# Kernel tuning notes

Measured on AMD Instinct MI355X. Metric: run time of the kernel, lower is better.

The kernel has to match this reference:

```python
import jax, jax.numpy as jnp
import numpy as np
from jax import lax

BN_EPS = 1e-5  # eval-mode BatchNorm with running_mean=0, running_var=1


def _interp_mat(n_in, n_out):
    # align_corners=True bilinear interpolation matrix [n_out, n_in]
    if n_out == 1:
        coords = np.zeros((1,))
    else:
        coords = np.arange(n_out) * (n_in - 1) / (n_out - 1)
    lo = np.clip(np.floor(coords).astype(np.int64), 0, max(n_in - 2, 0))
    frac = (coords - lo).astype(np.float32)
    M = np.zeros((n_out, n_in), dtype=np.float32)
    M[np.arange(n_out), lo] += 1.0 - frac
    if n_in > 1:
        M[np.arange(n_out), lo + 1] += frac
    return jnp.asarray(M)


def _resize_ac(x, H, W):
    # bilinear, align_corners=True, over trailing two dims
    Mh = _interp_mat(x.shape[-2], H)
    Mw = _interp_mat(x.shape[-1], W)
    return jnp.einsum('...hw,Hh,Ww->...HW', x, Mh, Mw)


def _conv(x, w, b, pad):
    y = lax.conv_general_dilated(x, w, (1, 1), [(pad, pad), (pad, pad)],
                                 dimension_numbers=('NCHW', 'OIHW', 'NCHW'))
    return y + b[None, :, None, None]


def setup_inputs() -> dict:
    key = jax.random.key(0)
    ks = jax.random.split(key, 16)
    C, KD, VD, NCLS, BS = 256, 32, 128, 10, 4
    sizes = [64, 32, 16, 8, 4]
    inp = {}
    for l, s in enumerate(sizes):
        inp[f'feat{l}'] = jax.random.normal(ks[l], (BS, C, s, s), jnp.float32)
    inp['attentions'] = jax.random.normal(ks[5], (NCLS, C, 16, 16), jnp.float32)

    def w(k, shape):
        return jax.random.normal(k, shape, jnp.float32) * 0.05

    inp['key_t_w'] = w(ks[6], (KD, C, 3, 3)); inp['key_t_b'] = jnp.zeros((KD,), jnp.float32)
    inp['value_t_w'] = w(ks[7], (VD, C, 3, 3)); inp['value_t_b'] = jnp.zeros((VD,), jnp.float32)
    inp['key_q_w'] = w(ks[8], (5, KD, C, 3, 3)); inp['key_q_b'] = jnp.zeros((5, KD), jnp.float32)
    inp['value_q_w'] = w(ks[9], (5, VD, C, 3, 3)); inp['value_q_b'] = jnp.zeros((5, VD), jnp.float32)
    inp['bn_gamma'] = jnp.ones((5, 256), jnp.float32)
    inp['bn_beta'] = jnp.zeros((5, 256), jnp.float32)
    inp['combine_w'] = w(ks[10], (256, 512, 1, 1)); inp['combine_b'] = jnp.zeros((256,), jnp.float32)
    return inp


def reference(feat0, feat1, feat2, feat3, feat4, attentions,
              key_t_w, key_t_b, value_t_w, value_t_b,
              key_q_w, key_q_b, value_q_w, value_q_b,
              bn_gamma, bn_beta, combine_w, combine_b):
    feats = [feat0, feat1, feat2, feat3, feat4]
    ncls, _, h, w_ = attentions.shape
    hw = h * w_
    kt = _conv(attentions, key_t_w, key_t_b, 1).reshape(ncls, 32, hw)   # [n,32,hw]
    vt = _conv(attentions, value_t_w, value_t_b, 1).reshape(ncls, 128, hw)  # [n,128,hw]
    bn_scale = bn_gamma * np.float32(1.0 / np.sqrt(1.0 + BN_EPS))
    outs, fas = [], []
    for l, f in enumerate(feats):
        bs, _, H, W = f.shape
        fr = _resize_ac(f, h, w_)                                        # [b,C,h,w]
        kq = _conv(fr, key_q_w[l], key_q_b[l], 1).reshape(bs, 32, hw)    # [b,32,hw]
        vq = _conv(fr, value_q_w[l], value_q_b[l], 1)                    # [b,128,h,w]
        # p[b,n,i,j] = sum_k kq[b,k,i] * kt[n,k,j]; softmax over i (torch dim=1)
        p = jnp.einsum('bki,nkj->bnij', kq, kt)
        p = jax.nn.softmax(p, axis=2)
        # full attention maps: channels = template pixel j, spatial = query pixel i
        fa = _resize_ac(jnp.swapaxes(p, 2, 3).reshape(bs, ncls, hw, h, w_), H, W)
        # val_t_out summed over classes: sum_n sum_i vt[n,c,i] * p[b,n,i,j]
        agg = jnp.einsum('nci,bnij->bcj', vt, p).reshape(bs, 128, h, w_)
        final = jnp.concatenate([ncls * vq, agg], axis=1)                # [b,256,h,w]
        final = _resize_ac(final, H, W)
        final = final * bn_scale[l][None, :, None, None] + bn_beta[l][None, :, None, None]
        outs.append(_conv(jnp.concatenate([f, final], axis=1), combine_w, combine_b, 0))
        fas.append(fa)
    return (*outs, *fas)
```

## Files before the change

kernel.cpp:

```cpp
#include <hip/hip_runtime.h>

constexpr int CIN   = 256;
constexpr int KD    = 32;
constexpr int VD    = 128;
constexpr int NCLS  = 10;
constexpr int BS    = 4;
constexpr int HW    = 256;
constexpr float BNC = 0.9999950000374997f;

typedef unsigned short u16;
typedef __attribute__((ext_vector_type(8))) __bf16 bf8v;
typedef __attribute__((ext_vector_type(4))) float f4v;

static __device__ __forceinline__ int imin(int a, int b) { return a < b ? a : b; }

static __device__ __forceinline__ u16 f2bf(float v) {
  union { float f; unsigned u; } x; x.f = v;
  unsigned r = x.u + 0x7FFFu + ((x.u >> 16) & 1u);
  return (u16)(r >> 16);
}
static __device__ __forceinline__ float bf2f(u16 h) {
  union { unsigned u; float f; } x; x.u = ((unsigned)h) << 16;
  return x.f;
}

static __device__ __forceinline__ f4v mfma16(bf8v a, bf8v b, f4v c) {
  return __builtin_amdgcn_mfma_f32_16x16x32_bf16(a, b, c, 0, 0, 0);
}

__constant__ const int c_jbase[5] = {0, 16384, 20480, 21504, 21760};

__global__ __launch_bounds__(256) void k_prep_f(
    const float* __restrict__ f0, const float* __restrict__ f1,
    const float* __restrict__ f2, const float* __restrict__ f3,
    const float* __restrict__ f4, const float* __restrict__ att,
    u16* __restrict__ Xf, u16* __restrict__ Xr) {
  int blk = blockIdx.x;
  const float* fin; u16* dstbase; int SS, px0;
  if (blk < 344) {
    int l, base, nb;
    if (blk < 256)      { l = 0; base = 0;   nb = 64; }
    else if (blk < 320) { l = 1; base = 256; nb = 16; }
    else if (blk < 336) { l = 2; base = 320; nb = 4; }
    else if (blk < 340) { l = 3; base = 336; nb = 1; }
    else                { l = 4; base = 340; nb = 1; }
    int local = blk - base;
    int b = local / nb, chunk = local % nb;
    int S = 64 >> l; SS = S * S;
    px0 = chunk * 64;
    fin = (l == 0 ? f0 : l == 1 ? f1 : l == 2 ? f2 : l == 3 ? f3 : f4)
          + (size_t)b * CIN * SS;
    dstbase = Xf + (size_t)(c_jbase[l] + b * SS) * 512;
  } else {
    int a = blk - 344;
    int imgA = a >> 2, chunk = a & 3;
    SS = 256; px0 = chunk * 64;
    fin = att + (size_t)imgA * CIN * 256;
    dstbase = Xr + (size_t)(20 + imgA) * 131072;
  }
  int tid = threadIdx.x;
  __shared__ float sm[16][65];
  int px_r = tid & 63, cr = tid >> 6;
  int px_w = tid >> 2, c4 = (tid & 3) * 4;
  for (int cbk = 0; cbk < 16; ++cbk) {
    __syncthreads();
#pragma unroll
    for (int q = 0; q < 4; ++q) {
      int cl = q * 4 + cr;
      float v = 0.f;
      if (px0 + px_r < SS) v = fin[(size_t)(cbk * 16 + cl) * SS + px0 + px_r];
      sm[cl][px_r] = v;
    }
    __syncthreads();
    if (px0 + px_w < SS) {
      u16 hh[4], ll[4];
#pragma unroll
      for (int e = 0; e < 4; ++e) {
        float v = sm[c4 + e][px_w];
        hh[e] = f2bf(v); ll[e] = f2bf(v - bf2f(hh[e]));
      }
      uint2 wh, wl;
      wh.x = (unsigned)hh[0] | ((unsigned)hh[1] << 16); wh.y = (unsigned)hh[2] | ((unsigned)hh[3] << 16);
      wl.x = (unsigned)ll[0] | ((unsigned)ll[1] << 16); wl.y = (unsigned)ll[2] | ((unsigned)ll[3] << 16);
      u16* dst = dstbase + (size_t)(px0 + px_w) * 512 + cbk * 16 + c4;
      *reinterpret_cast<uint2*>(dst) = wh;
      *reinterpret_cast<uint2*>(dst + 256) = wl;
    }
  }
}

__global__ __launch_bounds__(256) void k_prep_xr(
    const u16* __restrict__ Xf, u16* __restrict__ Xr, u16* __restrict__ zrow) {
  int blk = blockIdx.x;
  int img = blk >> 4, yr = blk & 15;
  int l = img >> 2, b = img & 3;
  int S = 64 >> l, SS = S * S;
  int c = threadIdx.x;
  if (blk == 0) { zrow[c] = 0; zrow[256 + c] = 0; }
  float cyf = (float)(yr * (S - 1)) / 15.0f;
  int ylo = imin((int)cyf, S - 2); float fy = cyf - (float)ylo;
  u16* dst = Xr + ((size_t)img * 256 + yr * 16) * 512;
  const u16* srcb = Xf + (size_t)(c_jbase[l] + b * SS) * 512;
  for (int x = 0; x < 16; ++x) {
    float cxf = (float)(x * (S - 1)) / 15.0f;
    int xlo = imin((int)cxf, S - 2); float fx = cxf - (float)xlo;
    const u16* r00 = srcb + (size_t)(ylo * S + xlo) * 512;
    const u16* r10 = srcb + (size_t)((ylo + 1) * S + xlo) * 512;
    float v00 = bf2f(r00[c]) + bf2f(r00[256 + c]);
    float v01 = bf2f(r00[512 + c]) + bf2f(r00[768 + c]);
    float v10 = bf2f(r10[c]) + bf2f(r10[256 + c]);
    float v11 = bf2f(r10[512 + c]) + bf2f(r10[768 + c]);
    float v = (1.f - fy) * ((1.f - fx) * v00 + fx * v01)
            + fy * ((1.f - fx) * v10 + fx * v11);
    u16 h = f2bf(v);
    dst[x * 512 + c] = h;
    dst[x * 512 + 256 + c] = f2bf(v - bf2f(h));
  }
}

__global__ __launch_bounds__(256) void k_prep_w(
    const float* __restrict__ vqw, const float* __restrict__ vtw,
    const float* __restrict__ kqw, const float* __restrict__ ktw,
    u16* __restrict__ Awv, u16* __restrict__ Awk) {
  int gid = blockIdx.x * 256 + threadIdx.x;
  int lane = gid & 63;
  int grp = gid >> 6;
  const float* src; u16* dst; int kc;
  if (grp < 3456) {
    kc = grp % 72; int ot = (grp / 72) % 8; int sid = grp / (72 * 8);
    src = (sid < 5 ? vqw + (size_t)sid * VD * 2304 : vtw) + (size_t)(ot * 16 + (lane & 15)) * 2304;
    dst = Awv + (size_t)grp * 1024;
  } else {
    int g2 = grp - 3456;
    kc = g2 % 72; int ot = (g2 / 72) % 2; int sid = g2 / 144;
    src = (sid < 5 ? kqw + (size_t)sid * KD * 2304 : ktw) + (size_t)(ot * 16 + (lane & 15)) * 2304;
    dst = Awk + (size_t)g2 * 1024;
  }
  int q0 = (lane >> 4) * 8;
  int t = kc >> 3, c0 = (kc & 7) * 32;
#pragma unroll
  for (int i = 0; i < 8; ++i) {
    int c = c0 + q0 + i;
    float v = src[c * 9 + t];
    u16 h = f2bf(v);
    dst[lane * 8 + i] = h;
    dst[512 + lane * 8 + i] = f2bf(v - bf2f(h));
  }
}

__global__ __launch_bounds__(256) void k_prep_cwg(
    const float* __restrict__ cw, const float* __restrict__ gamma,
    u16* __restrict__ cwA, u16* __restrict__ cw2A) {
  int blk = blockIdx.x;
  if (blk < 64) {
    int gid = blk * 256 + threadIdx.x;
    int oc = gid >> 6, c0 = (gid & 63) * 4;
    float4 v = *reinterpret_cast<const float4*>(cw + (size_t)oc * 512 + c0);
    const float* vv = (const float*)&v;
    u16 h[4], l[4];
#pragma unroll
    for (int e = 0; e < 4; ++e) { h[e] = f2bf(vv[e]); l[e] = f2bf(vv[e] - bf2f(h[e])); }
    uint2 wh, wl;
    wh.x = (unsigned)h[0] | ((unsigned)h[1] << 16); wh.y = (unsigned)h[2] | ((unsigned)h[3] << 16);
    wl.x = (unsigned)l[0] | ((unsigned)l[1] << 16); wl.y = (unsigned)l[2] | ((unsigned)l[3] << 16);
    *reinterpret_cast<uint2*>(cwA + (size_t)oc * 256 + c0) = wh;
    *reinterpret_cast<uint2*>(cwA + 65536 + (size_t)oc * 256 + c0) = wl;
  } else {
    int gid = (blk - 64) * 256 + threadIdx.x;
    int l = gid / 16384, rem = gid % 16384;
    int oc = rem >> 6, c0 = (rem & 63) * 4;
    u16 h[4], lo[4];
#pragma unroll
    for (int e = 0; e < 4; ++e) {
      int c = c0 + e;
      float v = cw[(size_t)oc * 512 + 256 + c] * (gamma[l * 256 + c] * BNC);
      h[e] = f2bf(v); lo[e] = f2bf(v - bf2f(h[e]));
    }
    uint2 wh, wl;
    wh.x = (unsigned)h[0] | ((unsigned)h[1] << 16); wh.y = (unsigned)h[2] | ((unsigned)h[3] << 16);
    wl.x = (unsigned)lo[0] | ((unsigned)lo[1] << 16); wl.y = (unsigned)lo[2] | ((unsigned)lo[3] << 16);
    *reinterpret_cast<uint2*>(cw2A + (size_t)l * 65536 + oc * 256 + c0) = wh;
    *reinterpret_cast<uint2*>(cw2A + 327680 + (size_t)l * 65536 + oc * 256 + c0) = wl;
  }
}

__global__ __launch_bounds__(256) void k_cb(
    const float* __restrict__ cw, const float* __restrict__ cbias,
    const float* __restrict__ beta, float* __restrict__ cb) {
  int l = blockIdx.x, oc = threadIdx.x;
  float s = cbias[oc];
  for (int c = 0; c < CIN; ++c)
    s += cw[(size_t)oc * 512 + 256 + c] * beta[l * CIN + c];
  cb[l * CIN + oc] = s;
}

__global__ __launch_bounds__(256) void k_conv_mfma(
    const u16* __restrict__ Xr, const u16* __restrict__ Awv, const u16* __restrict__ Awk,
    const u16* __restrict__ zrow,
    float* __restrict__ kqall, float* __restrict__ vt, float* __restrict__ f16v,
    const float* __restrict__ vqb, const float* __restrict__ vtb,
    const float* __restrict__ kqb, const float* __restrict__ ktb) {
  int wid = blockIdx.x * 4 + (threadIdx.x >> 6);
  int lane = threadIdx.x & 63;
  bool isV = wid < 1920;
  int img, ot, yp;
  if (isV) { img = wid >> 6; int r = wid & 63; ot = r >> 3; yp = r & 7; }
  else     { int j = wid - 1920; img = j >> 4; int r = j & 15; ot = r >> 3; yp = r & 7; }
  int wset = img < 20 ? (img >> 2) : 5;

  const u16* Ab = isV ? Awv + ((size_t)(wset * 8 + ot)) * 72 * 1024
                      : Awk + ((size_t)(wset * 2 + ot)) * 72 * 1024;
  const u16* Xb = Xr + (size_t)img * 131072;
  int xcol = lane & 15, kg = lane >> 4;
  int y0 = yp * 2, y1 = y0 + 1;

  f4v acc0 = {0.f, 0.f, 0.f, 0.f}, acc1 = {0.f, 0.f, 0.f, 0.f};
  for (int t = 0; t < 9; ++t) {
    int dy = (t >= 6) ? 2 : (t >= 3 ? 1 : 0);
    int dx = t - dy * 3;
    int yy0 = y0 + dy - 1, yy1 = yy0 + 1;
    int xx = xcol + dx - 1;
    bool xok = (unsigned)xx < 16u;
    const u16* base0 = (xok && (unsigned)yy0 < 16u)
                       ? Xb + (size_t)(yy0 * 16 + xx) * 512 : zrow;
    const u16* base1 = (xok && (unsigned)yy1 < 16u)
                       ? Xb + (size_t)(yy1 * 16 + xx) * 512 : zrow;
    const u16* Xr0 = base0 + kg * 8;
    const u16* Xr1 = base1 + kg * 8;
    const u16* Ak = Ab + (size_t)t * 8 * 1024 + lane * 8;
#pragma unroll
    for (int cc = 0; cc < 8; ++cc) {
      bf8v ah = *reinterpret_cast<const bf8v*>(Ak + cc * 1024);
      bf8v al = *reinterpret_cast<const bf8v*>(Ak + cc * 1024 + 512);
      bf8v bh0 = *reinterpret_cast<const bf8v*>(Xr0 + cc * 32);
      bf8v bl0 = *reinterpret_cast<const bf8v*>(Xr0 + cc * 32 + 256);
      bf8v bh1 = *reinterpret_cast<const bf8v*>(Xr1 + cc * 32);
      bf8v bl1 = *reinterpret_cast<const bf8v*>(Xr1 + cc * 32 + 256);
      acc0 = mfma16(ah, bh0, acc0);
      acc0 = mfma16(ah, bl0, acc0);
      acc0 = mfma16(al, bh0, acc0);
      acc1 = mfma16(ah, bh1, acc1);
      acc1 = mfma16(ah, bl1, acc1);
      acc1 = mfma16(al, bh1, acc1);
    }
  }

  float scale = 1.f;
  const float* bias;
  float* dst;
  int ocbase = ot * 16;
  if (isV) {
    if (img < 20) { dst = f16v + ((size_t)img * VD + ocbase) * HW; bias = vqb + wset * VD + ocbase; scale = (float)NCLS; }
    else          { dst = vt + ((size_t)(img - 20) * VD + ocbase) * HW; bias = vtb + ocbase; }
  } else {
    if (img < 20) { dst = kqall + ((size_t)img * KD + ocbase) * HW; bias = kqb + wset * KD + ocbase; }
    else          { dst = kqall + (size_t)20 * KD * HW + ((size_t)(img - 20) * KD + ocbase) * HW; bias = ktb + ocbase; }
  }
#pragma unroll
  for (int i = 0; i < 4; ++i) {
    int ocl = kg * 4 + i;
    float bv = bias[ocl];
    dst[(size_t)ocl * HW + y0 * 16 + xcol] = (acc0[i] + bv) * scale;
    dst[(size_t)ocl * HW + y1 * 16 + xcol] = (acc1[i] + bv) * scale;
  }
}

__global__ __launch_bounds__(256) void k_prep_vt(
    const float* __restrict__ vt, u16* __restrict__ vt2) {
  int gid = blockIdx.x * 256 + threadIdx.x;
  float4 v = *reinterpret_cast<const float4*>(vt + (size_t)gid * 4);
  const float* vv = (const float*)&v;
  u16 h[4], l[4];
#pragma unroll
  for (int e = 0; e < 4; ++e) { h[e] = f2bf(vv[e]); l[e] = f2bf(vv[e] - bf2f(h[e])); }
  uint2 wh, wl;
  wh.x = (unsigned)h[0] | ((unsigned)h[1] << 16); wh.y = (unsigned)h[2] | ((unsigned)h[3] << 16);
  wl.x = (unsigned)l[0] | ((unsigned)l[1] << 16); wl.y = (unsigned)l[2] | ((unsigned)l[3] << 16);
  *reinterpret_cast<uint2*>(vt2 + (size_t)gid * 4) = wh;
  *reinterpret_cast<uint2*>(vt2 + 327680 + (size_t)gid * 4) = wl;
}

__global__ __launch_bounds__(256) void k_mega(
    const float* __restrict__ kqall, const u16* __restrict__ vt2,
    float* __restrict__ out, float* __restrict__ aggn) {
  int blk = blockIdx.x;
  int l = blk / 160;
  int r = blk % 160;
  int b = r / 40;
  int r2 = r % 40;
  int np = r2 >> 3, jt = r2 & 7;
  int t = threadIdx.x;
  int iq = t >> 5, jl = t & 31;
  int j = jt * 32 + jl;

  __shared__ float buf[8224];
  __shared__ float red[512];

  const float* ktb = kqall + 20 * KD * HW;
  const float* kqb = kqall + (size_t)(l * 4 + b) * KD * HW;

  int S_ = 64 >> l, shift = 6 - l, SS = S_ * S_;
  const size_t fa_off[5] = {5586944, 47529984, 58015744, 60637184, 61292544};

  int w = t >> 6, lane = t & 63;
  int row = lane & 15, kg = lane >> 4;
  f4v acc[2][2] = {{{0.f,0.f,0.f,0.f},{0.f,0.f,0.f,0.f}},
                   {{0.f,0.f,0.f,0.f},{0.f,0.f,0.f,0.f}}};

  for (int half = 0; half < 2; ++half) {
    int n = np * 2 + half;
    int bn = b * NCLS + n;
    __syncthreads();
    for (int s = t; s < KD * HW; s += 256) buf[s] = kqb[s];
    float ktr[KD];
#pragma unroll
    for (int k = 0; k < KD; ++k) ktr[k] = ktb[((size_t)n * KD + k) * HW + j];
    __syncthreads();

    float v[32];
#pragma unroll
    for (int ii = 0; ii < 32; ++ii) v[ii] = 0.f;
    for (int k = 0; k < KD; ++k) {
      float a = ktr[k];
      const float4* q4 = (const float4*)&buf[k * 256 + iq * 32];
#pragma unroll
      for (int q = 0; q < 8; ++q) {
        float4 u = q4[q];
        v[q * 4 + 0] += u.x * a; v[q * 4 + 1] += u.y * a;
        v[q * 4 + 2] += u.z * a; v[q * 4 + 3] += u.w * a;
      }
    }
    float ml = -1e30f;
#pragma unroll
    for (int ii = 0; ii < 32; ++ii) ml = fmaxf(ml, v[ii]);
    float sl = 0.f;
#pragma unroll
    for (int ii = 0; ii < 32; ++ii) sl += __expf(v[ii] - ml);
    red[t] = ml;
    red[256 + t] = sl;
    __syncthreads();
    float M = -1e30f;
#pragma unroll
    for (int q = 0; q < 8; ++q) M = fmaxf(M, red[q * 32 + jl]);
    float Ssum = 0.f;
#pragma unroll
    for (int q = 0; q < 8; ++q) Ssum += red[256 + q * 32 + jl] * __expf(red[q * 32 + jl] - M);
    float inv = 1.0f / Ssum;
#pragma unroll
    for (int ii = 0; ii < 32; ++ii)
      buf[jl * 257 + iq * 32 + ii] = __expf(v[ii] - M) * inv;
    __syncthreads();

    float* ob = out + fa_off[l] + ((size_t)bn * HW + jt * 32) * SS;
    int tot = SS << 5;
    for (int base = t * 4; base < tot; base += 1024) {
      int jj = base >> (2 * shift);
      int rest = base & (SS - 1);
      int X0 = rest & (S_ - 1), Y = rest >> shift;
      float cyf = (float)(Y * 15) / (float)(S_ - 1);
      int ylo = imin((int)cyf, 14); float fy = cyf - (float)ylo;
      const float* prow = &buf[jj * 257];
      float4 rv; float* rr = (float*)&rv;
#pragma unroll
      for (int t4 = 0; t4 < 4; ++t4) {
        int X = X0 + t4;
        float cxf = (float)(X * 15) / (float)(S_ - 1);
        int xlo = imin((int)cxf, 14); float fx = cxf - (float)xlo;
        int i00 = ylo * 16 + xlo;
        float v0 = prow[i00],      v1 = prow[i00 + 1];
        float v2 = prow[i00 + 16], v3 = prow[i00 + 17];
        rr[t4] = (1.f - fy) * ((1.f - fx) * v0 + fx * v1)
               + fy * ((1.f - fx) * v2 + fx * v3);
      }
      *(float4*)(ob + (size_t)jj * SS + rest) = rv;
    }

    for (int kc = 0; kc < 8; ++kc) {
      bf8v ah[2], al[2];
#pragma unroll
      for (int ctl = 0; ctl < 2; ++ctl) {
        int ct = w * 2 + ctl;
        const u16* vh = vt2 + ((size_t)n * VD + ct * 16 + row) * 256 + kc * 32 + kg * 8;
        ah[ctl] = *reinterpret_cast<const bf8v*>(vh);
        al[ctl] = *reinterpret_cast<const bf8v*>(vh + 327680);
      }
#pragma unroll
      for (int jt2 = 0; jt2 < 2; ++jt2) {
        union { u16 u[8]; bf8v v8; } Bh, Bl;
#pragma unroll
        for (int e = 0; e < 8; ++e) {
          float f = buf[(jt2 * 16 + row) * 257 + kc * 32 + kg * 8 + e];
          u16 h = f2bf(f);
          Bh.u[e] = h; Bl.u[e] = f2bf(f - bf2f(h));
        }
#pragma unroll
        for (int ctl = 0; ctl < 2; ++ctl) {
          acc[ctl][jt2] = mfma16(ah[ctl], Bh.v8, acc[ctl][jt2]);
          acc[ctl][jt2] = mfma16(ah[ctl], Bl.v8, acc[ctl][jt2]);
          acc[ctl][jt2] = mfma16(al[ctl], Bh.v8, acc[ctl][jt2]);
        }
      }
    }
  }

  float* ab = aggn + (size_t)(l * 20 + b * 5 + np) * VD * HW;
#pragma unroll
  for (int ctl = 0; ctl < 2; ++ctl)
#pragma unroll
    for (int jt2 = 0; jt2 < 2; ++jt2)
#pragma unroll
      for (int i = 0; i < 4; ++i)
        ab[(size_t)(w * 32 + ctl * 16 + kg * 4 + i) * HW + jt * 32 + jt2 * 16 + row]
            = acc[ctl][jt2][i];
}

__global__ __launch_bounds__(256) void k_fuse_fs(
    const float* __restrict__ f16v, const float* __restrict__ aggn,
    u16* __restrict__ fsT) {
  int blk = blockIdx.x;
  int img = blk >> 4, jc = blk & 15;
  int j0 = jc * 16;
  int l = img >> 2, b = img & 3;
  int tid = threadIdx.x;
  __shared__ float fs[256][17];
  for (int pass = 0; pass < 16; ++pass) {
    int cc = pass * 16 + (tid >> 4);
    int jj = tid & 15;
    float v;
    if (cc < 128) {
      v = f16v[((size_t)img * VD + cc) * HW + j0 + jj];
    } else {
      const float* ab = aggn + ((size_t)(l * 20 + b * 5) * VD + cc - 128) * HW + j0 + jj;
      v = 0.f;
#pragma unroll
      for (int npx = 0; npx < 5; ++npx) v += ab[(size_t)npx * VD * HW];
    }
    fs[cc][jj] = v;
  }
  __syncthreads();
  int j = tid >> 4, cg = (tid & 15) * 16;
  u16* dst = fsT + ((size_t)img * 256 + j0 + j) * 512 + cg;
#pragma unroll
  for (int e = 0; e < 16; ++e) {
    float v = fs[cg + e][j];
    u16 h = f2bf(v);
    dst[e] = h;
    dst[256 + e] = f2bf(v - bf2f(h));
  }
}

__global__ __launch_bounds__(256) void k_g16_mfma(
    const u16* __restrict__ cw2A, const u16* __restrict__ fsT,
    float* __restrict__ g16_all) {
  int wid = blockIdx.x * 4 + (threadIdx.x >> 6);
  int lane = threadIdx.x & 63;
  int img = wid >> 8;
  int r = wid & 255;
  int octile = r >> 4, jt = r & 15;
  int l = img >> 2;
  int row = lane & 15, kg = lane >> 4;
  const u16* Ah = cw2A + (size_t)l * 65536 + (octile * 16 + row) * 256 + kg * 8;
  const u16* Al = Ah + 327680;
  const u16* Bh = fsT + ((size_t)img * 256 + jt * 16 + row) * 512 + kg * 8;
  const u16* Bl = Bh + 256;
  f4v acc = {0.f, 0.f, 0.f, 0.f};
#pragma unroll
  for (int kc = 0; kc < 8; ++kc) {
    bf8v ah = *reinterpret_cast<const bf8v*>(Ah + kc * 32);
    bf8v al = *reinterpret_cast<const bf8v*>(Al + kc * 32);
    bf8v bh = *reinterpret_cast<const bf8v*>(Bh + kc * 32);
    bf8v bl = *reinterpret_cast<const bf8v*>(Bl + kc * 32);
    acc = mfma16(ah, bh, acc);
    acc = mfma16(ah, bl, acc);
    acc = mfma16(al, bh, acc);
  }
#pragma unroll
  for (int i = 0; i < 4; ++i)
    g16_all[((size_t)img * CIN + octile * 16 + kg * 4 + i) * HW + jt * 16 + row] = acc[i];
}

__global__ __launch_bounds__(256) void k_out_final(
    const u16* __restrict__ cwA, const u16* __restrict__ Xf,
    const float* __restrict__ g16_all, const float* __restrict__ cb_all,
    float* __restrict__ out) {
  int wid = blockIdx.x * 4 + (threadIdx.x >> 6);
  int lane = threadIdx.x & 63;
  int pt = wid >> 4, octile = wid & 15;
  int l, lb, tl;
  if (pt < 1024)      { l = 0; lb = 0;    tl = 256; }
  else if (pt < 1280) { l = 1; lb = 1024; tl = 64; }
  else if (pt < 1344) { l = 2; lb = 1280; tl = 16; }
  else if (pt < 1360) { l = 3; lb = 1344; tl = 4; }
  else                { l = 4; lb = 1360; tl = 1; }
  int rem = pt - lb;
  int b = rem / tl;
  int pxin = (rem % tl) * 16;
  const size_t ooff[5] = {0, 4194304, 5242880, 5505024, 5570560};
  int S = 64 >> l, SS = S * S, shift = 6 - l;
  int row = lane & 15, kg = lane >> 4;
  int gpx = c_jbase[l] + b * SS + pxin + row;

  const u16* Ah = cwA + ((size_t)(octile * 16 + row)) * 256 + kg * 8;
  const u16* Al = Ah + 65536;
  const u16* Bh = Xf + (size_t)gpx * 512 + kg * 8;
  const u16* Bl = Bh + 256;
  f4v acc = {0.f, 0.f, 0.f, 0.f};
#pragma unroll
  for (int kc = 0; kc < 8; ++kc) {
    bf8v ah = *reinterpret_cast<const bf8v*>(Ah + kc * 32);
    bf8v al = *reinterpret_cast<const bf8v*>(Al + kc * 32);
    bf8v bh = *reinterpret_cast<const bf8v*>(Bh + kc * 32);
    bf8v bl = *reinterpret_cast<const bf8v*>(Bl + kc * 32);
    acc = mfma16(ah, bh, acc);
    acc = mfma16(ah, bl, acc);
    acc = mfma16(al, bh, acc);
  }

  int px = pxin + row;
  int Xc = px & (S - 1), Y = px >> shift;
  float cyf = (float)(Y * 15) / (float)(S - 1);
  int ylo = imin((int)cyf, 14); float fy = cyf - (float)ylo;
  float cxf = (float)(Xc * 15) / (float)(S - 1);
  int xlo = imin((int)cxf, 14); float fx = cxf - (float)xlo;
  int i00 = ylo * 16 + xlo;
  const float* gbase = g16_all + ((size_t)(l * 4 + b) * CIN + octile * 16 + kg * 4) * HW;
  float* ob = out + ooff[l] + ((size_t)b * CIN + octile * 16) * SS + px;
#pragma unroll
  for (int i = 0; i < 4; ++i) {
    const float* g = gbase + (size_t)i * HW + i00;
    float v0 = g[0], v1 = g[1], v2 = g[16], v3 = g[17];
    float bil = (1.f - fy) * ((1.f - fx) * v0 + fx * v1)
              + fy * ((1.f - fx) * v2 + fx * v3);
    ob[(size_t)(kg * 4 + i) * SS] = acc[i] + bil + cb_all[l * CIN + octile * 16 + kg * 4 + i];
  }
}

extern "C" void kernel_launch(void* const* d_in, const int* in_sizes, int n_in,
                              void* d_out, int out_size, void* d_ws, size_t ws_size,
                              hipStream_t stream) {
  const float* feat[5];
  for (int l = 0; l < 5; ++l) feat[l] = (const float*)d_in[l];
  const float* att   = (const float*)d_in[5];
  const float* ktw   = (const float*)d_in[6];
  const float* ktb   = (const float*)d_in[7];
  const float* vtw   = (const float*)d_in[8];
  const float* vtb   = (const float*)d_in[9];
  const float* kqw   = (const float*)d_in[10];
  const float* kqb   = (const float*)d_in[11];
  const float* vqw   = (const float*)d_in[12];
  const float* vqb   = (const float*)d_in[13];
  const float* gamma = (const float*)d_in[14];
  const float* beta  = (const float*)d_in[15];
  const float* cw    = (const float*)d_in[16];
  const float* cbias = (const float*)d_in[17];
  float* out = (float*)d_out;

  float* ws    = (float*)d_ws;
  float* kqall = ws;
  float* f16v  = ws + 245760;
  u16*   vt2   = (u16*)(ws + 901120);
  u16*   cwA   = (u16*)(ws + 1228800);
  u16*   cw2A  = (u16*)(ws + 1294336);
  float* cb    = ws + 1622016;
  u16*   Xf    = (u16*)(ws + 1623296);
  float* S0    = ws + 7210240;
  u16*   Awv  = (u16*)S0;
  u16*   Awk  = (u16*)(S0 + 1769472);
  u16*   Xr   = (u16*)(S0 + 2211840);
  float* vt   = S0 + 4177920;
  u16*   zrow = (u16*)(S0 + 4505600);
  float* aggn    = S0;
  u16*   fsT     = (u16*)(S0 + 3276800);
  float* g16_all = S0;

  k_prep_f<<<384, 256, 0, stream>>>(
      feat[0], feat[1], feat[2], feat[3], feat[4], att, Xf, Xr);
  k_prep_w<<<1080, 256, 0, stream>>>(vqw, vtw, kqw, ktw, Awv, Awk);
  k_prep_cwg<<<384, 256, 0, stream>>>(cw, gamma, cwA, cw2A);
  k_cb<<<5, 256, 0, stream>>>(cw, cbias, beta, cb);
  k_prep_xr<<<320, 256, 0, stream>>>(Xf, Xr, zrow);
  k_conv_mfma<<<600, 256, 0, stream>>>(
      Xr, Awv, Awk, zrow, kqall, vt, f16v, vqb, vtb, kqb, ktb);
  k_prep_vt<<<320, 256, 0, stream>>>(vt, vt2);

  k_mega<<<800, 256, 0, stream>>>(kqall, vt2, out, aggn);
  k_fuse_fs<<<320, 256, 0, stream>>>(f16v, aggn, fsT);

  k_g16_mfma<<<1280, 256, 0, stream>>>(cw2A, fsT, g16_all);
  k_out_final<<<5456, 256, 0, stream>>>(cwA, Xf, g16_all, cb, out);
}
```

Baseline: 403.5 us.

## Merge prep kernels, fuse vt split into conv epilogue, one class per mega block

Four weight and feature prep kernels are merged into one launch, and the separate fp32-to-bf16 hi/lo split of the template values is moved into the conv epilogue, which drops a kernel and an intermediate buffer. k_mega now handles one class per block with twice as many blocks instead of looping over two classes, giving more parallelism. The cost is a larger aggn buffer (10 partial sums per image instead of 5) that k_fuse_fs must read and reduce, which adds memory traffic and requires moving the workspace layout.

```diff
diff --git a/kernel.cpp b/kernel.cpp
--- a/kernel.cpp
+++ b/kernel.cpp
@@ -30,62 +30,133 @@
 
 __constant__ const int c_jbase[5] = {0, 16384, 20480, 21504, 21760};
 
-__global__ __launch_bounds__(256) void k_prep_f(
+__global__ __launch_bounds__(256) void k_prep1(
     const float* __restrict__ f0, const float* __restrict__ f1,
     const float* __restrict__ f2, const float* __restrict__ f3,
     const float* __restrict__ f4, const float* __restrict__ att,
-    u16* __restrict__ Xf, u16* __restrict__ Xr) {
+    const float* __restrict__ vqw, const float* __restrict__ vtw,
+    const float* __restrict__ kqw, const float* __restrict__ ktw,
+    const float* __restrict__ cw, const float* __restrict__ gamma,
+    const float* __restrict__ cbias, const float* __restrict__ beta,
+    u16* __restrict__ Xf, u16* __restrict__ Xr,
+    u16* __restrict__ Awv, u16* __restrict__ Awk,
+    u16* __restrict__ cwA, u16* __restrict__ cw2A, float* __restrict__ cb) {
+  __shared__ float sm[16][65];
   int blk = blockIdx.x;
-  const float* fin; u16* dstbase; int SS, px0;
-  if (blk < 344) {
-    int l, base, nb;
-    if (blk < 256)      { l = 0; base = 0;   nb = 64; }
-    else if (blk < 320) { l = 1; base = 256; nb = 16; }
-    else if (blk < 336) { l = 2; base = 320; nb = 4; }
-    else if (blk < 340) { l = 3; base = 336; nb = 1; }
-    else                { l = 4; base = 340; nb = 1; }
-    int local = blk - base;
-    int b = local / nb, chunk = local % nb;
-    int S = 64 >> l; SS = S * S;
-    px0 = chunk * 64;
-    fin = (l == 0 ? f0 : l == 1 ? f1 : l == 2 ? f2 : l == 3 ? f3 : f4)
-          + (size_t)b * CIN * SS;
-    dstbase = Xf + (size_t)(c_jbase[l] + b * SS) * 512;
-  } else {
-    int a = blk - 344;
-    int imgA = a >> 2, chunk = a & 3;
-    SS = 256; px0 = chunk * 64;
-    fin = att + (size_t)imgA * CIN * 256;
-    dstbase = Xr + (size_t)(20 + imgA) * 131072;
-  }
   int tid = threadIdx.x;
-  __shared__ float sm[16][65];
-  int px_r = tid & 63, cr = tid >> 6;
-  int px_w = tid >> 2, c4 = (tid & 3) * 4;
-  for (int cbk = 0; cbk < 16; ++cbk) {
-    __syncthreads();
-#pragma unroll
-    for (int q = 0; q < 4; ++q) {
-      int cl = q * 4 + cr;
-      float v = 0.f;
-      if (px0 + px_r < SS) v = fin[(size_t)(cbk * 16 + cl) * SS + px0 + px_r];
-      sm[cl][px_r] = v;
-    }
-    __syncthreads();
-    if (px0 + px_w < SS) {
-      u16 hh[4], ll[4];
+  if (blk < 384) {
+    const float* fin; u16* dstbase; int SS, px0;
+    if (blk < 344) {
+      int l, base, nb;
+      if (blk < 256)      { l = 0; base = 0;   nb = 64; }
+      else if (blk < 320) { l = 1; base = 256; nb = 16; }
+      else if (blk < 336) { l = 2; base = 320; nb = 4; }
+      else if (blk < 340) { l = 3; base = 336; nb = 1; }
+      else                { l = 4; base = 340; nb = 1; }
+      int local = blk - base;
+      int b = local / nb, chunk = local % nb;
+      int S = 64 >> l; SS = S * S;
+      px0 = chunk * 64;
+      fin = (l == 0 ? f0 : l == 1 ? f1 : l == 2 ? f2 : l == 3 ? f3 : f4)
+            + (size_t)b * CIN * SS;
+      dstbase = Xf + (size_t)(c_jbase[l] + b * SS) * 512;
+    } else {
+      int a = blk - 344;
+      int imgA = a >> 2, chunk = a & 3;
+      SS = 256; px0 = chunk * 64;
+      fin = att + (size_t)imgA * CIN * 256;
+      dstbase = Xr + (size_t)(20 + imgA) * 131072;
+    }
+    int px_r = tid & 63, cr = tid >> 6;
+    int px_w = tid >> 2, c4 = (tid & 3) * 4;
+    for (int cbk = 0; cbk < 16; ++cbk) {
+      __syncthreads();
+#pragma unroll
+      for (int q = 0; q < 4; ++q) {
+        int cl = q * 4 + cr;
+        float v = 0.f;
+        if (px0 + px_r < SS) v = fin[(size_t)(cbk * 16 + cl) * SS + px0 + px_r];
+        sm[cl][px_r] = v;
+      }
+      __syncthreads();
+      if (px0 + px_w < SS) {
+        u16 hh[4], ll[4];
+#pragma unroll
+        for (int e = 0; e < 4; ++e) {
+          float v = sm[c4 + e][px_w];
+          hh[e] = f2bf(v); ll[e] = f2bf(v - bf2f(hh[e]));
+        }
+        uint2 wh, wl;
+        wh.x = (unsigned)hh[0] | ((unsigned)hh[1] << 16); wh.y = (unsigned)hh[2] | ((unsigned)hh[3] << 16);
+        wl.x = (unsigned)ll[0] | ((unsigned)ll[1] << 16); wl.y = (unsigned)ll[2] | ((unsigned)ll[3] << 16);
+        u16* dst = dstbase + (size_t)(px0 + px_w) * 512 + cbk * 16 + c4;
+        *reinterpret_cast<uint2*>(dst) = wh;
+        *reinterpret_cast<uint2*>(dst + 256) = wl;
+      }
+    }
+  } else if (blk < 1464) {
+    int gid = (blk - 384) * 256 + tid;
+    int lane = gid & 63;
+    int grp = gid >> 6;
+    const float* src; u16* dst; int kc;
+    if (grp < 3456) {
+      kc = grp % 72; int ot = (grp / 72) % 8; int sid = grp / (72 * 8);
+      src = (sid < 5 ? vqw + (size_t)sid * VD * 2304 : vtw) + (size_t)(ot * 16 + (lane & 15)) * 2304;
+      dst = Awv + (size_t)grp * 1024;
+    } else {
+      int g2 = grp - 3456;
+      kc = g2 % 72; int ot = (g2 / 72) % 2; int sid = g2 / 144;
+      src = (sid < 5 ? kqw + (size_t)sid * KD * 2304 : ktw) + (size_t)(ot * 16 + (lane & 15)) * 2304;
+      dst = Awk + (size_t)g2 * 1024;
+    }
+    int q0 = (lane >> 4) * 8;
+    int t = kc >> 3, c0 = (kc & 7) * 32;
+#pragma unroll
+    for (int i = 0; i < 8; ++i) {
+      int c = c0 + q0 + i;
+      float v = src[c * 9 + t];
+      u16 h = f2bf(v);
+      dst[lane * 8 + i] = h;
+      dst[512 + lane * 8 + i] = f2bf(v - bf2f(h));
+    }
+  } else if (blk < 1848) {
+    int blk2 = blk - 1464;
+    if (blk2 < 64) {
+      int gid = blk2 * 256 + tid;
+      int oc = gid >> 6, c0 = (gid & 63) * 4;
+      float4 v = *reinterpret_cast<const float4*>(cw + (size_t)oc * 512 + c0);
+      const float* vv = (const float*)&v;
+      u16 h[4], l[4];
+#pragma unroll
+      for (int e = 0; e < 4; ++e) { h[e] = f2bf(vv[e]); l[e] = f2bf(vv[e] - bf2f(h[e])); }
+      uint2 wh, wl;
+      wh.x = (unsigned)h[0] | ((unsigned)h[1] << 16); wh.y = (unsigned)h[2] | ((unsigned)h[3] << 16);
+      wl.x = (unsigned)l[0] | ((unsigned)l[1] << 16); wl.y = (unsigned)l[2] | ((unsigned)l[3] << 16);
+      *reinterpret_cast<uint2*>(cwA + (size_t)oc * 256 + c0) = wh;
+      *reinterpret_cast<uint2*>(cwA + 65536 + (size_t)oc * 256 + c0) = wl;
+    } else {
+      int gid = (blk2 - 64) * 256 + tid;
+      int l = gid / 16384, rem = gid % 16384;
+      int oc = rem >> 6, c0 = (rem & 63) * 4;
+      u16 h[4], lo[4];
 #pragma unroll
       for (int e = 0; e < 4; ++e) {
-        float v = sm[c4 + e][px_w];
-        hh[e] = f2bf(v); ll[e] = f2bf(v - bf2f(hh[e]));
+        int c = c0 + e;
+        float v = cw[(size_t)oc * 512 + 256 + c] * (gamma[l * 256 + c] * BNC);
+        h[e] = f2bf(v); lo[e] = f2bf(v - bf2f(h[e]));
       }
       uint2 wh, wl;
-      wh.x = (unsigned)hh[0] | ((unsigned)hh[1] << 16); wh.y = (unsigned)hh[2] | ((unsigned)hh[3] << 16);
-      wl.x = (unsigned)ll[0] | ((unsigned)ll[1] << 16); wl.y = (unsigned)ll[2] | ((unsigned)ll[3] << 16);
-      u16* dst = dstbase + (size_t)(px0 + px_w) * 512 + cbk * 16 + c4;
-      *reinterpret_cast<uint2*>(dst) = wh;
-      *reinterpret_cast<uint2*>(dst + 256) = wl;
-    }
+      wh.x = (unsigned)h[0] | ((unsigned)h[1] << 16); wh.y = (unsigned)h[2] | ((unsigned)h[3] << 16);
+      wl.x = (unsigned)lo[0] | ((unsigned)lo[1] << 16); wl.y = (unsigned)lo[2] | ((unsigned)lo[3] << 16);
+      *reinterpret_cast<uint2*>(cw2A + (size_t)l * 65536 + oc * 256 + c0) = wh;
+      *reinterpret_cast<uint2*>(cw2A + 327680 + (size_t)l * 65536 + oc * 256 + c0) = wl;
+    }
+  } else {
+    int l = blk - 1848, oc = tid;
+    float s = cbias[oc];
+    for (int c = 0; c < CIN; ++c)
+      s += cw[(size_t)oc * 512 + 256 + c] * beta[l * CIN + c];
+    cb[l * CIN + oc] = s;
   }
 }
 
@@ -118,86 +189,10 @@
   }
 }
 
-__global__ __launch_bounds__(256) void k_prep_w(
-    const float* __restrict__ vqw, const float* __restrict__ vtw,
-    const float* __restrict__ kqw, const float* __restrict__ ktw,
-    u16* __restrict__ Awv, u16* __restrict__ Awk) {
-  int gid = blockIdx.x * 256 + threadIdx.x;
-  int lane = gid & 63;
-  int grp = gid >> 6;
-  const float* src; u16* dst; int kc;
-  if (grp < 3456) {
-    kc = grp % 72; int ot = (grp / 72) % 8; int sid = grp / (72 * 8);
-    src = (sid < 5 ? vqw + (size_t)sid * VD * 2304 : vtw) + (size_t)(ot * 16 + (lane & 15)) * 2304;
-    dst = Awv + (size_t)grp * 1024;
-  } else {
-    int g2 = grp - 3456;
-    kc = g2 % 72; int ot = (g2 / 72) % 2; int sid = g2 / 144;
-    src = (sid < 5 ? kqw + (size_t)sid * KD * 2304 : ktw) + (size_t)(ot * 16 + (lane & 15)) * 2304;
-    dst = Awk + (size_t)g2 * 1024;
-  }
-  int q0 = (lane >> 4) * 8;
-  int t = kc >> 3, c0 = (kc & 7) * 32;
-#pragma unroll
-  for (int i = 0; i < 8; ++i) {
-    int c = c0 + q0 + i;
-    float v = src[c * 9 + t];
-    u16 h = f2bf(v);
-    dst[lane * 8 + i] = h;
-    dst[512 + lane * 8 + i] = f2bf(v - bf2f(h));
-  }
-}
-
-__global__ __launch_bounds__(256) void k_prep_cwg(
-    const float* __restrict__ cw, const float* __restrict__ gamma,
-    u16* __restrict__ cwA, u16* __restrict__ cw2A) {
-  int blk = blockIdx.x;
-  if (blk < 64) {
-    int gid = blk * 256 + threadIdx.x;
-    int oc = gid >> 6, c0 = (gid & 63) * 4;
-    float4 v = *reinterpret_cast<const float4*>(cw + (size_t)oc * 512 + c0);
-    const float* vv = (const float*)&v;
-    u16 h[4], l[4];
-#pragma unroll
-    for (int e = 0; e < 4; ++e) { h[e] = f2bf(vv[e]); l[e] = f2bf(vv[e] - bf2f(h[e])); }
-    uint2 wh, wl;
-    wh.x = (unsigned)h[0] | ((unsigned)h[1] << 16); wh.y = (unsigned)h[2] | ((unsigned)h[3] << 16);
-    wl.x = (unsigned)l[0] | ((unsigned)l[1] << 16); wl.y = (unsigned)l[2] | ((unsigned)l[3] << 16);
-    *reinterpret_cast<uint2*>(cwA + (size_t)oc * 256 + c0) = wh;
-    *reinterpret_cast<uint2*>(cwA + 65536 + (size_t)oc * 256 + c0) = wl;
-  } else {
-    int gid = (blk - 64) * 256 + threadIdx.x;
-    int l = gid / 16384, rem = gid % 16384;
-    int oc = rem >> 6, c0 = (rem & 63) * 4;
-    u16 h[4], lo[4];
-#pragma unroll
-    for (int e = 0; e < 4; ++e) {
-      int c = c0 + e;
-      float v = cw[(size_t)oc * 512 + 256 + c] * (gamma[l * 256 + c] * BNC);
-      h[e] = f2bf(v); lo[e] = f2bf(v - bf2f(h[e]));
-    }
-    uint2 wh, wl;
-    wh.x = (unsigned)h[0] | ((unsigned)h[1] << 16); wh.y = (unsigned)h[2] | ((unsigned)h[3] << 16);
-    wl.x = (unsigned)lo[0] | ((unsigned)lo[1] << 16); wl.y = (unsigned)lo[2] | ((unsigned)lo[3] << 16);
-    *reinterpret_cast<uint2*>(cw2A + (size_t)l * 65536 + oc * 256 + c0) = wh;
-    *reinterpret_cast<uint2*>(cw2A + 327680 + (size_t)l * 65536 + oc * 256 + c0) = wl;
-  }
-}
-
-__global__ __launch_bounds__(256) void k_cb(
-    const float* __restrict__ cw, const float* __restrict__ cbias,
-    const float* __restrict__ beta, float* __restrict__ cb) {
-  int l = blockIdx.x, oc = threadIdx.x;
-  float s = cbias[oc];
-  for (int c = 0; c < CIN; ++c)
-    s += cw[(size_t)oc * 512 + 256 + c] * beta[l * CIN + c];
-  cb[l * CIN + oc] = s;
-}
-
 __global__ __launch_bounds__(256) void k_conv_mfma(
     const u16* __restrict__ Xr, const u16* __restrict__ Awv, const u16* __restrict__ Awk,
     const u16* __restrict__ zrow,
-    float* __restrict__ kqall, float* __restrict__ vt, float* __restrict__ f16v,
+    float* __restrict__ kqall, u16* __restrict__ vt2, float* __restrict__ f16v,
     const float* __restrict__ vqb, const float* __restrict__ vtb,
     const float* __restrict__ kqb, const float* __restrict__ ktb) {
   int wid = blockIdx.x * 4 + (threadIdx.x >> 6);
@@ -245,17 +240,29 @@
     }
   }
 
+  int ocbase = ot * 16;
+  if (isV && img >= 20) {
+    int n = img - 20;
+    u16* d2 = vt2 + ((size_t)n * VD + ocbase) * HW;
+#pragma unroll
+    for (int i = 0; i < 4; ++i) {
+      int ocl = kg * 4 + i;
+      float bv = vtb[ocbase + ocl];
+      float va = acc0[i] + bv, vb = acc1[i] + bv;
+      u16 ha = f2bf(va), hb = f2bf(vb);
+      size_t ia = (size_t)ocl * HW + y0 * 16 + xcol;
+      size_t ib = (size_t)ocl * HW + y1 * 16 + xcol;
+      d2[ia] = ha; d2[ia + 327680] = f2bf(va - bf2f(ha));
+      d2[ib] = hb; d2[ib + 327680] = f2bf(vb - bf2f(hb));
+    }
+    return;
+  }
   float scale = 1.f;
   const float* bias;
   float* dst;
-  int ocbase = ot * 16;
-  if (isV) {
-    if (img < 20) { dst = f16v + ((size_t)img * VD + ocbase) * HW; bias = vqb + wset * VD + ocbase; scale = (float)NCLS; }
-    else          { dst = vt + ((size_t)(img - 20) * VD + ocbase) * HW; bias = vtb + ocbase; }
-  } else {
-    if (img < 20) { dst = kqall + ((size_t)img * KD + ocbase) * HW; bias = kqb + wset * KD + ocbase; }
-    else          { dst = kqall + (size_t)20 * KD * HW + ((size_t)(img - 20) * KD + ocbase) * HW; bias = ktb + ocbase; }
-  }
+  if (isV) { dst = f16v + ((size_t)img * VD + ocbase) * HW; bias = vqb + wset * VD + ocbase; scale = (float)NCLS; }
+  else if (img < 20) { dst = kqall + ((size_t)img * KD + ocbase) * HW; bias = kqb + wset * KD + ocbase; }
+  else { dst = kqall + (size_t)20 * KD * HW + ((size_t)(img - 20) * KD + ocbase) * HW; bias = ktb + ocbase; }
 #pragma unroll
   for (int i = 0; i < 4; ++i) {
     int ocl = kg * 4 + i;
@@ -265,30 +272,14 @@
   }
 }
 
-__global__ __launch_bounds__(256) void k_prep_vt(
-    const float* __restrict__ vt, u16* __restrict__ vt2) {
-  int gid = blockIdx.x * 256 + threadIdx.x;
-  float4 v = *reinterpret_cast<const float4*>(vt + (size_t)gid * 4);
-  const float* vv = (const float*)&v;
-  u16 h[4], l[4];
-#pragma unroll
-  for (int e = 0; e < 4; ++e) { h[e] = f2bf(vv[e]); l[e] = f2bf(vv[e] - bf2f(h[e])); }
-  uint2 wh, wl;
-  wh.x = (unsigned)h[0] | ((unsigned)h[1] << 16); wh.y = (unsigned)h[2] | ((unsigned)h[3] << 16);
-  wl.x = (unsigned)l[0] | ((unsigned)l[1] << 16); wl.y = (unsigned)l[2] | ((unsigned)l[3] << 16);
-  *reinterpret_cast<uint2*>(vt2 + (size_t)gid * 4) = wh;
-  *reinterpret_cast<uint2*>(vt2 + 327680 + (size_t)gid * 4) = wl;
-}
-
 __global__ __launch_bounds__(256) void k_mega(
     const float* __restrict__ kqall, const u16* __restrict__ vt2,
     float* __restrict__ out, float* __restrict__ aggn) {
   int blk = blockIdx.x;
-  int l = blk / 160;
-  int r = blk % 160;
-  int b = r / 40;
-  int r2 = r % 40;
-  int np = r2 >> 3, jt = r2 & 7;
+  int l = blk / 320;
+  int r = blk % 320;
+  int bn = r >> 3, jt = r & 7;
+  int b = bn / NCLS, n = bn % NCLS;
   int t = threadIdx.x;
   int iq = t >> 5, jl = t & 31;
   int j = jt * 32 + jl;
@@ -297,113 +288,104 @@
   __shared__ float red[512];
 
   const float* ktb = kqall + 20 * KD * HW;
+  float ktr[KD];
+#pragma unroll
+  for (int k = 0; k < KD; ++k) ktr[k] = ktb[((size_t)n * KD + k) * HW + j];
   const float* kqb = kqall + (size_t)(l * 4 + b) * KD * HW;
+  for (int s = t; s < KD * HW; s += 256) buf[s] = kqb[s];
+  __syncthreads();
+
+  float v[32];
+#pragma unroll
+  for (int ii = 0; ii < 32; ++ii) v[ii] = 0.f;
+  for (int k = 0; k < KD; ++k) {
+    float a = ktr[k];
+    const float4* q4 = (const float4*)&buf[k * 256 + iq * 32];
+#pragma unroll
+    for (int q = 0; q < 8; ++q) {
+      float4 u = q4[q];
+      v[q * 4 + 0] += u.x * a; v[q * 4 + 1] += u.y * a;
+      v[q * 4 + 2] += u.z * a; v[q * 4 + 3] += u.w * a;
+    }
+  }
+  float ml = -1e30f;
+#pragma unroll
+  for (int ii = 0; ii < 32; ++ii) ml = fmaxf(ml, v[ii]);
+  float sl = 0.f;
+#pragma unroll
+  for (int ii = 0; ii < 32; ++ii) sl += __expf(v[ii] - ml);
+  red[t] = ml;
+  red[256 + t] = sl;
+  __syncthreads();
+  float M = -1e30f;
+#pragma unroll
+  for (int q = 0; q < 8; ++q) M = fmaxf(M, red[q * 32 + jl]);
+  float Ssum = 0.f;
+#pragma unroll
+  for (int q = 0; q < 8; ++q) Ssum += red[256 + q * 32 + jl] * __expf(red[q * 32 + jl] - M);
+  float inv = 1.0f / Ssum;
+#pragma unroll
+  for (int ii = 0; ii < 32; ++ii)
+    buf[jl * 257 + iq * 32 + ii] = __expf(v[ii] - M) * inv;
+  __syncthreads();
 
   int S_ = 64 >> l, shift = 6 - l, SS = S_ * S_;
   const size_t fa_off[5] = {5586944, 47529984, 58015744, 60637184, 61292544};
+  float* ob = out + fa_off[l] + ((size_t)bn * HW + jt * 32) * SS;
+  int tot = SS << 5;
+  for (int base = t * 4; base < tot; base += 1024) {
+    int jj = base >> (2 * shift);
+    int rest = base & (SS - 1);
+    int X0 = rest & (S_ - 1), Y = rest >> shift;
+    float cyf = (float)(Y * 15) / (float)(S_ - 1);
+    int ylo = imin((int)cyf, 14); float fy = cyf - (float)ylo;
+    const float* prow = &buf[jj * 257];
+    float4 rv; float* rr = (float*)&rv;
+#pragma unroll
+    for (int t4 = 0; t4 < 4; ++t4) {
+      int X = X0 + t4;
+      float cxf = (float)(X * 15) / (float)(S_ - 1);
+      int xlo = imin((int)cxf, 14); float fx = cxf - (float)xlo;
+      int i00 = ylo * 16 + xlo;
+      float v0 = prow[i00],      v1 = prow[i00 + 1];
+      float v2 = prow[i00 + 16], v3 = prow[i00 + 17];
+      rr[t4] = (1.f - fy) * ((1.f - fx) * v0 + fx * v1)
+             + fy * ((1.f - fx) * v2 + fx * v3);
+    }
+    *(float4*)(ob + (size_t)jj * SS + rest) = rv;
+  }
 
   int w = t >> 6, lane = t & 63;
   int row = lane & 15, kg = lane >> 4;
   f4v acc[2][2] = {{{0.f,0.f,0.f,0.f},{0.f,0.f,0.f,0.f}},
                    {{0.f,0.f,0.f,0.f},{0.f,0.f,0.f,0.f}}};
-
-  for (int half = 0; half < 2; ++half) {
-    int n = np * 2 + half;
-    int bn = b * NCLS + n;
-    __syncthreads();
-    for (int s = t; s < KD * HW; s += 256) buf[s] = kqb[s];
-    float ktr[KD];
-#pragma unroll
-    for (int k = 0; k < KD; ++k) ktr[k] = ktb[((size_t)n * KD + k) * HW + j];
-    __syncthreads();
-
-    float v[32];
-#pragma unroll
-    for (int ii = 0; ii < 32; ++ii) v[ii] = 0.f;
-    for (int k = 0; k < KD; ++k) {
-      float a = ktr[k];
-      const float4* q4 = (const float4*)&buf[k * 256 + iq * 32];
-#pragma unroll
-      for (int q = 0; q < 8; ++q) {
-        float4 u = q4[q];
-        v[q * 4 + 0] += u.x * a; v[q * 4 + 1] += u.y * a;
-        v[q * 4 + 2] += u.z * a; v[q * 4 + 3] += u.w * a;
+  for (int kc = 0; kc < 8; ++kc) {
+    bf8v ah[2], al[2];
+#pragma unroll
+    for (int ctl = 0; ctl < 2; ++ctl) {
+      int ct = w * 2 + ctl;
+      const u16* vh = vt2 + ((size_t)n * VD + ct * 16 + row) * 256 + kc * 32 + kg * 8;
+      ah[ctl] = *reinterpret_cast<const bf8v*>(vh);
+      al[ctl] = *reinterpret_cast<const bf8v*>(vh + 327680);
+    }
+#pragma unroll
+    for (int jt2 = 0; jt2 < 2; ++jt2) {
+      union { u16 u[8]; bf8v v8; } Bh, Bl;
+#pragma unroll
+      for (int e = 0; e < 8; ++e) {
+        float f = buf[(jt2 * 16 + row) * 257 + kc * 32 + kg * 8 + e];
+        u16 h = f2bf(f);
+        Bh.u[e] = h; Bl.u[e] = f2bf(f - bf2f(h));
       }
-    }
-    float ml = -1e30f;
-#pragma unroll
-    for (int ii = 0; ii < 32; ++ii) ml = fmaxf(ml, v[ii]);
-    float sl = 0.f;
-#pragma unroll
-    for (int ii = 0; ii < 32; ++ii) sl += __expf(v[ii] - ml);
-    red[t] = ml;
-    red[256 + t] = sl;
-    __syncthreads();
-    float M = -1e30f;
-#pragma unroll
-    for (int q = 0; q < 8; ++q) M = fmaxf(M, red[q * 32 + jl]);
-    float Ssum = 0.f;
-#pragma unroll
-    for (int q = 0; q < 8; ++q) Ssum += red[256 + q * 32 + jl] * __expf(red[q * 32 + jl] - M);
-    float inv = 1.0f / Ssum;
-#pragma unroll
-    for (int ii = 0; ii < 32; ++ii)
-      buf[jl * 257 + iq * 32 + ii] = __expf(v[ii] - M) * inv;
-    __syncthreads();
-
-    float* ob = out + fa_off[l] + ((size_t)bn * HW + jt * 32) * SS;
-    int tot = SS << 5;
-    for (int base = t * 4; base < tot; base += 1024) {
-      int jj = base >> (2 * shift);
-      int rest = base & (SS - 1);
-      int X0 = rest & (S_ - 1), Y = rest >> shift;
-      float cyf = (float)(Y * 15) / (float)(S_ - 1);
-      int ylo = imin((int)cyf, 14); float fy = cyf - (float)ylo;
-      const float* prow = &buf[jj * 257];
-      float4 rv; float* rr = (float*)&rv;
-#pragma unroll
-      for (int t4 = 0; t4 < 4; ++t4) {
-        int X = X0 + t4;
-        float cxf = (float)(X * 15) / (float)(S_ - 1);
-        int xlo = imin((int)cxf, 14); float fx = cxf - (float)xlo;
-        int i00 = ylo * 16 + xlo;
-        float v0 = prow[i00],      v1 = prow[i00 + 1];
-        float v2 = prow[i00 + 16], v3 = prow[i00 + 17];
-        rr[t4] = (1.f - fy) * ((1.f - fx) * v0 + fx * v1)
-               + fy * ((1.f - fx) * v2 + fx * v3);
+#pragma unroll
+      for (int ctl = 0; ctl < 2; ++ctl) {
+        acc[ctl][jt2] = mfma16(ah[ctl], Bh.v8, acc[ctl][jt2]);
+        acc[ctl][jt2] = mfma16(ah[ctl], Bl.v8, acc[ctl][jt2]);
+        acc[ctl][jt2] = mfma16(al[ctl], Bh.v8, acc[ctl][jt2]);
       }
-      *(float4*)(ob + (size_t)jj * SS + rest) = rv;
-    }
-
-    for (int kc = 0; kc < 8; ++kc) {
-      bf8v ah[2], al[2];
-#pragma unroll
-      for (int ctl = 0; ctl < 2; ++ctl) {
-        int ct = w * 2 + ctl;
-        const u16* vh = vt2 + ((size_t)n * VD + ct * 16 + row) * 256 + kc * 32 + kg * 8;
-        ah[ctl] = *reinterpret_cast<const bf8v*>(vh);
-        al[ctl] = *reinterpret_cast<const bf8v*>(vh + 327680);
-      }
-#pragma unroll
-      for (int jt2 = 0; jt2 < 2; ++jt2) {
-        union { u16 u[8]; bf8v v8; } Bh, Bl;
-#pragma unroll
-        for (int e = 0; e < 8; ++e) {
-          float f = buf[(jt2 * 16 + row) * 257 + kc * 32 + kg * 8 + e];
-          u16 h = f2bf(f);
-          Bh.u[e] = h; Bl.u[e] = f2bf(f - bf2f(h));
-        }
-#pragma unroll
-        for (int ctl = 0; ctl < 2; ++ctl) {
-          acc[ctl][jt2] = mfma16(ah[ctl], Bh.v8, acc[ctl][jt2]);
-          acc[ctl][jt2] = mfma16(ah[ctl], Bl.v8, acc[ctl][jt2]);
-          acc[ctl][jt2] = mfma16(al[ctl], Bh.v8, acc[ctl][jt2]);
-        }
-      }
-    }
-  }
-
-  float* ab = aggn + (size_t)(l * 20 + b * 5 + np) * VD * HW;
+    }
+  }
+  float* ab = aggn + (size_t)(l * 40 + bn) * VD * HW;
 #pragma unroll
   for (int ctl = 0; ctl < 2; ++ctl)
 #pragma unroll
@@ -430,10 +412,10 @@
     if (cc < 128) {
       v = f16v[((size_t)img * VD + cc) * HW + j0 + jj];
     } else {
-      const float* ab = aggn + ((size_t)(l * 20 + b * 5) * VD + cc - 128) * HW + j0 + jj;
+      const float* ab = aggn + ((size_t)(l * 40 + b * 10) * VD + cc - 128) * HW + j0 + jj;
       v = 0.f;
 #pragma unroll
-      for (int npx = 0; npx < 5; ++npx) v += ab[(size_t)npx * VD * HW];
+      for (int n = 0; n < NCLS; ++n) v += ab[(size_t)n * VD * HW];
     }
     fs[cc][jj] = v;
   }
@@ -567,23 +549,20 @@
   u16*   Awv  = (u16*)S0;
   u16*   Awk  = (u16*)(S0 + 1769472);
   u16*   Xr   = (u16*)(S0 + 2211840);
-  float* vt   = S0 + 4177920;
-  u16*   zrow = (u16*)(S0 + 4505600);
+  u16*   zrow = (u16*)(S0 + 4177920);
   float* aggn    = S0;
-  u16*   fsT     = (u16*)(S0 + 3276800);
+  u16*   fsT     = (u16*)(S0 + 6553600);
   float* g16_all = S0;
 
-  k_prep_f<<<384, 256, 0, stream>>>(
-      feat[0], feat[1], feat[2], feat[3], feat[4], att, Xf, Xr);
-  k_prep_w<<<1080, 256, 0, stream>>>(vqw, vtw, kqw, ktw, Awv, Awk);
-  k_prep_cwg<<<384, 256, 0, stream>>>(cw, gamma, cwA, cw2A);
-  k_cb<<<5, 256, 0, stream>>>(cw, cbias, beta, cb);
+  k_prep1<<<1853, 256, 0, stream>>>(
+      feat[0], feat[1], feat[2], feat[3], feat[4], att,
+      vqw, vtw, kqw, ktw, cw, gamma, cbias, beta,
+      Xf, Xr, Awv, Awk, cwA, cw2A, cb);
   k_prep_xr<<<320, 256, 0, stream>>>(Xf, Xr, zrow);
   k_conv_mfma<<<600, 256, 0, stream>>>(
-      Xr, Awv, Awk, zrow, kqall, vt, f16v, vqb, vtb, kqb, ktb);
-  k_prep_vt<<<320, 256, 0, stream>>>(vt, vt2);
-
-  k_mega<<<800, 256, 0, stream>>>(kqall, vt2, out, aggn);
+      Xr, Awv, Awk, zrow, kqall, vt2, f16v, vqb, vtb, kqb, ktb);
+
+  k_mega<<<1600, 256, 0, stream>>>(kqall, vt2, out, aggn);
   k_fuse_fs<<<320, 256, 0, stream>>>(f16v, aggn, fsT);
 
   k_g16_mfma<<<1280, 256, 0, stream>>>(cw2A, fsT, g16_all);
```

Measured after the change: 363.8 us. -9.8%, faster.
